# Kernel tuning notes

Measured on AMD Instinct MI355X. Metric: run time of the kernel, lower is better.

Reference implementation:

```python
import jax, jax.numpy as jnp
import numpy as np

EPS = 1e-5
SLOPE = 0.2
K = 20
B, N = 8, 2048

def _lrelu(x):
    return jnp.where(x >= 0, x, SLOPE * x)

def _bn(x, g, b, m, v, axis):
    # eval-mode batchnorm with running stats
    shape = [1] * x.ndim
    shape[axis] = -1
    g, b, m, v = (t.reshape(shape) for t in (g, b, m, v))
    return g * (x - m) * jax.lax.rsqrt(v + EPS) + b

def _knn(x, k):
    # x: (B, C, N) -> neighbor indices (B, N, k) by largest negative sq dist
    xx = jnp.sum(x * x, axis=1)                      # (B, N)
    inner = jnp.einsum('bcn,bcm->bnm', x, x)         # (B, N, N)
    pd = 2.0 * inner - xx[:, :, None] - xx[:, None, :]
    return jax.lax.top_k(pd, k)[1]

def _graph_feature(x, k):
    # x: (B, C, N) -> (B, 2C, N, k) edge features [nbr - center, center]
    idx = _knn(x, k)                                  # (B, N, k)
    xt = jnp.transpose(x, (0, 2, 1))                  # (B, N, C)
    nbr = xt[jnp.arange(x.shape[0])[:, None, None], idx]  # (B, N, k, C)
    center = xt[:, :, None, :]
    f = jnp.concatenate([nbr - center, jnp.broadcast_to(center, nbr.shape)], axis=-1)
    return jnp.transpose(f, (0, 3, 1, 2))

def _edge_block(x, W, g, b, m, v):
    f = _graph_feature(x, K)                          # (B, 2C, N, k)
    h = jnp.einsum('oc,bcnk->bonk', W, f)             # 1x1 conv
    return jnp.max(_lrelu(_bn(h, g, b, m, v, 1)), axis=-1)

def _forward(x, W1, bn1_g, bn1_b, bn1_m, bn1_v, W2, bn2_g, bn2_b, bn2_m, bn2_v, W3, bn3_g, bn3_b, bn3_m, bn3_v, W4, bn4_g, bn4_b, bn4_m, bn4_v, l1_w, l1_b, bn5_g, bn5_b, bn5_m, bn5_v, l2_w, l2_b, bn6_g, bn6_b, bn6_m, bn6_v, l3_w, l3_b):
    xc = jnp.transpose(x, (0, 2, 1))                  # (B, 3, N)
    x1 = _edge_block(xc, W1, bn1_g, bn1_b, bn1_m, bn1_v)   # (B, 64, N)
    x2 = _edge_block(x1, W2, bn2_g, bn2_b, bn2_m, bn2_v)   # (B, 64, N)
    x3 = _edge_block(x2, W3, bn3_g, bn3_b, bn3_m, bn3_v)   # (B, 128, N)
    h = jnp.concatenate([x1, x2, x3], axis=1)         # (B, 256, N)
    h = _lrelu(_bn(jnp.einsum('oc,bcn->bon', W4, h), bn4_g, bn4_b, bn4_m, bn4_v, 1))
    h = jnp.max(h, axis=-1)                           # (B, 1024)
    h = _lrelu(_bn(h @ l1_w.T + l1_b, bn5_g, bn5_b, bn5_m, bn5_v, 1))
    h = _lrelu(_bn(h @ l2_w.T + l2_b, bn6_g, bn6_b, bn6_m, bn6_v, 1))
    return h @ l3_w.T + l3_b                          # (B, 2)

def setup_inputs() -> dict:
    key = jax.random.key(0)
    ks = iter(jax.random.split(key, 64))
    def rn(shape, s=1.0):
        return jax.random.normal(next(ks), shape, jnp.float32) * s
    def add_bn(inp, prefix, c):
        inp[prefix + '_g'] = jax.random.uniform(next(ks), (c,), jnp.float32, 0.5, 1.5)
        inp[prefix + '_b'] = rn((c,), 0.1)
        inp[prefix + '_m'] = rn((c,), 0.1)
        inp[prefix + '_v'] = jax.random.uniform(next(ks), (c,), jnp.float32, 0.5, 1.5)
    inp = {'x': rn((B, N, 3))}
    inp['W1'] = rn((64, 6), 0.3); add_bn(inp, 'bn1', 64)
    inp['W2'] = rn((64, 128), 0.1); add_bn(inp, 'bn2', 64)
    inp['W3'] = rn((128, 128), 0.1); add_bn(inp, 'bn3', 128)
    inp['W4'] = rn((1024, 256), 0.08); add_bn(inp, 'bn4', 1024)
    inp['l1_w'] = rn((512, 1024), 0.03); inp['l1_b'] = rn((512,), 0.01); add_bn(inp, 'bn5', 512)
    inp['l2_w'] = rn((256, 512), 0.05); inp['l2_b'] = rn((256,), 0.01); add_bn(inp, 'bn6', 256)
    inp['l3_w'] = rn((2, 256), 0.06); inp['l3_b'] = rn((2,), 0.01)
    return inp

def reference(x, W1, bn1_g, bn1_b, bn1_m, bn1_v, W2, bn2_g, bn2_b, bn2_m, bn2_v, W3, bn3_g, bn3_b, bn3_m, bn3_v, W4, bn4_g, bn4_b, bn4_m, bn4_v, l1_w, l1_b, bn5_g, bn5_b, bn5_m, bn5_v, l2_w, l2_b, bn6_g, bn6_b, bn6_m, bn6_v, l3_w, l3_b):
    return _forward(x, W1, bn1_g, bn1_b, bn1_m, bn1_v, W2, bn2_g, bn2_b, bn2_m, bn2_v, W3, bn3_g, bn3_b, bn3_m, bn3_v, W4, bn4_g, bn4_b, bn4_m, bn4_v, l1_w, l1_b, bn5_g, bn5_b, bn5_m, bn5_v, l2_w, l2_b, bn6_g, bn6_b, bn6_m, bn6_v, l3_w, l3_b)
```

## Files before the change

kernel.cpp:

```cpp
#include <hip/hip_runtime.h>
#include <math.h>

#define NN 2048
#define KK 20
#define EPSF 1e-5f

__device__ __forceinline__ float lrelu(float v){ return v >= 0.f ? v : 0.2f*v; }

__device__ __forceinline__ void topk20_insert(float d, int idc, float (&v)[KK], int (&id)[KK]){
#pragma unroll
  for (int j = KK-1; j >= 1; --j){
    bool cjm1 = d > v[j-1];
    bool cj   = d > v[j];
    float nv = cjm1 ? v[j-1] : (cj ? d   : v[j]);
    int   ni = cjm1 ? id[j-1] : (cj ? idc : id[j]);
    v[j] = nv; id[j] = ni;
  }
  if (d > v[0]) { v[0] = d; id[0] = idc; }
}

__global__ void k_prep1(const float* __restrict__ x, const float* __restrict__ W1,
                        float* __restrict__ Y, float* __restrict__ T, float* __restrict__ SQ){
  __shared__ float wa[64][3], wd[64][3];
  int t = threadIdx.x;
  if (t < 64){
#pragma unroll
    for (int c=0;c<3;c++){
      float a = W1[t*6+c], b2 = W1[t*6+3+c];
      wa[t][c] = a; wd[t][c] = b2 - a;
    }
  }
  __syncthreads();
  int gid = blockIdx.x*256 + t;
  int b = gid >> 11, n = gid & (NN-1);
  float px = x[gid*3+0], py = x[gid*3+1], pz = x[gid*3+2];
  SQ[gid] = px*px + py*py + pz*pz;
  float* yb = Y + ((size_t)b*128)*NN + n;
  float* tb = T + ((size_t)b*128)*NN + n;
#pragma unroll 8
  for (int o=0;o<64;o++){
    yb[(size_t)o*NN] = wa[o][0]*px + wa[o][1]*py + wa[o][2]*pz;
    tb[(size_t)o*NN] = wd[o][0]*px + wd[o][1]*py + wd[o][2]*pz;
  }
}

__global__ __launch_bounds__(256) void k_knn3_part(const float* __restrict__ x, const float* __restrict__ SQ,
                                                   float* __restrict__ PV, unsigned short* __restrict__ PI){
  __shared__ __align__(16) float cd[128*4];
  int t = threadIdx.x;
  int half = blockIdx.x & 1, nb = blockIdx.x >> 1;
  int b = blockIdx.y;
  int n_base = nb * 32;
  int cbase = half * 1024;
  int ql = t & 31, sp = t >> 5;
  int n = n_base + ql;
  int gq = b*NN + n;
  float qx = x[gq*3], qy = x[gq*3+1], qz = x[gq*3+2];
  float qs = SQ[gq];
  float v[KK]; int id[KK];
#pragma unroll
  for (int i=0;i<KK;i++){ v[i] = -INFINITY; id[i] = 0; }
  int mlo = sp * 16;
  for (int tile=0; tile<8; ++tile){
    int m0 = cbase + tile * 128;
    __syncthreads();
#pragma unroll
    for (int i=0;i<2;i++){
      int f2 = t + i*256;
      int m = f2 >> 2, ch = f2 & 3;
      int gm = b*NN + m0 + m;
      cd[f2] = (ch < 3) ? x[gm*3 + ch] : SQ[gm];
    }
    __syncthreads();
    for (int j=mlo; j<mlo+16; ++j){
      float4 c4 = *(const float4*)&cd[j*4];
      float d = 2.f*(qx*c4.x + qy*c4.y + qz*c4.z) - qs - c4.w;
      if (d > v[KK-1]) topk20_insert(d, m0 + j, v, id);
    }
  }
  size_t base = ((size_t)b*16 + half*8 + sp)*KK;
#pragma unroll
  for (int r=0;r<KK;r++){
    PV[(base + r)*NN + n] = v[r];
    PI[(base + r)*NN + n] = (unsigned short)id[r];
  }
}

__global__ void k_sqnorm(const float* __restrict__ X, float* __restrict__ SQ){
  int gid = blockIdx.x*256 + threadIdx.x;
  int b = gid >> 11, n = gid & (NN-1);
  const float* xb = X + (size_t)b*256*NN;
  float s = 0.f;
#pragma unroll
  for (int c=0;c<64;c++){ float vv = xb[(size_t)c*NN + n]; s += vv*vv; }
  SQ[gid] = s;
}

__global__ __launch_bounds__(256) void k_gram(const float* __restrict__ X, float* __restrict__ D, int mh){
  __shared__ __align__(16) float am[32][132];
  __shared__ __align__(16) float bn[32][132];
  int t = threadIdx.x;
  int io = t >> 4, in_ = t & 15;
  int nb = blockIdx.x * 128;
  int mb = blockIdx.y * 128;
  int b = blockIdx.z;
  const float* xb = X + (size_t)b*256*NN;
  int mg = mh*1024 + mb;
  float acc[8][8];
#pragma unroll
  for (int r=0;r<8;r++)
#pragma unroll
    for (int c=0;c<8;c++) acc[r][c]=0.f;
  for (int c0=0; c0<64; c0+=32){
    __syncthreads();
#pragma unroll
    for (int p=0;p<4;p++){
      int idx = p*256 + t;
      int cc = idx >> 5, m4 = (idx & 31) * 4;
      *(float4*)&am[cc][m4] = *(const float4*)&xb[(size_t)(c0+cc)*NN + mg + m4];
    }
#pragma unroll
    for (int p=0;p<4;p++){
      int idx = p*256 + t;
      int cc = idx >> 5, n4 = (idx & 31) * 4;
      *(float4*)&bn[cc][n4] = *(const float4*)&xb[(size_t)(c0+cc)*NN + nb + n4];
    }
    __syncthreads();
#pragma unroll 4
    for (int c=0;c<32;c++){
      float4 a0 = *(const float4*)&am[c][io*8];
      float4 a1 = *(const float4*)&am[c][io*8+4];
      float4 b0 = *(const float4*)&bn[c][in_*8];
      float4 b1 = *(const float4*)&bn[c][in_*8+4];
      float ar[8] = {a0.x,a0.y,a0.z,a0.w,a1.x,a1.y,a1.z,a1.w};
      float br[8] = {b0.x,b0.y,b0.z,b0.w,b1.x,b1.y,b1.z,b1.w};
#pragma unroll
      for (int r=0;r<8;r++)
#pragma unroll
        for (int s=0;s<8;s++) acc[r][s] += ar[r]*br[s];
    }
  }
#pragma unroll
  for (int r=0;r<8;r++){
    size_t row = ((size_t)b*1024 + mb + io*8 + r)*NN + nb + in_*8;
    *(float4*)&D[row]   = make_float4(acc[r][0],acc[r][1],acc[r][2],acc[r][3]);
    *(float4*)&D[row+4] = make_float4(acc[r][4],acc[r][5],acc[r][6],acc[r][7]);
  }
}

__global__ __launch_bounds__(256) void k_sel1024(const float* __restrict__ D, const float* __restrict__ SQ,
                                                 int mh, float* __restrict__ PV, unsigned short* __restrict__ PI){
  int t = threadIdx.x;
  int q = t & 31, sp = t >> 5;
  int b = blockIdx.y;
  int n = blockIdx.x*32 + q;
  float qs = SQ[b*NN + n];
  const float* drow = D + ((size_t)b*1024 + sp*128)*NN + n;
  const float* sqb  = SQ + b*NN + mh*1024 + sp*128;
  int idb = mh*1024 + sp*128;
  float v[KK]; int id[KK];
#pragma unroll
  for (int i=0;i<KK;i++){ v[i]=-INFINITY; id[i]=0; }
  float dk[8];
#pragma unroll
  for (int k=0;k<8;k++) dk[k] = drow[(size_t)k*NN];
  for (int i=0;i<128;i+=8){
    float nk[8];
    if (i + 8 < 128){
#pragma unroll
      for (int k=0;k<8;k++) nk[k] = drow[(size_t)(i+8+k)*NN];
    }
#pragma unroll
    for (int k=0;k<8;k++){
      float d = 2.f*dk[k] - qs - sqb[i+k];
      if (d > v[KK-1]) topk20_insert(d, idb + i + k, v, id);
    }
#pragma unroll
    for (int k=0;k<8;k++) dk[k] = nk[k];
  }
  size_t base = ((size_t)b*16 + mh*8 + sp)*KK;
#pragma unroll
  for (int r=0;r<KK;r++){
    PV[(base + r)*NN + n] = v[r];
    PI[(base + r)*NN + n] = (unsigned short)id[r];
  }
}

__global__ void k_topk_merge16(const float* __restrict__ PV, const unsigned short* __restrict__ PI,
                               int* __restrict__ IDX){
  int gid = blockIdx.x*256 + threadIdx.x;
  int b = gid >> 11, n = gid & (NN-1);
  float hv[16]; int hi_[16]; int hp[16];
#pragma unroll
  for (int s=0;s<16;s++){
    hp[s] = 0;
    hv[s] = PV[(((size_t)b*16 + s)*KK)*NN + n];
    hi_[s] = (int)PI[(((size_t)b*16 + s)*KK)*NN + n];
  }
  for (int r=0;r<KK;r++){
    float bv = hv[0]; int bi = hi_[0]; int bs = 0;
#pragma unroll
    for (int s=1;s<16;s++){
      bool win = (hv[s] > bv) || ((hv[s] == bv) && (hi_[s] < bi));
      bv = win ? hv[s] : bv; bi = win ? hi_[s] : bi; bs = win ? s : bs;
    }
    IDX[((size_t)b*KK + r)*NN + n] = bi;
#pragma unroll
    for (int s=0;s<16;s++){
      if (s == bs){
        int np = hp[s] + 1; hp[s] = np;
        bool ok = np < KK;
        hv[s]  = ok ? PV[(((size_t)b*16 + s)*KK + np)*NN + n] : -INFINITY;
        hi_[s] = ok ? (int)PI[(((size_t)b*16 + s)*KK + np)*NN + n] : 0x7FFFFFFF;
      }
    }
  }
}

__global__ __launch_bounds__(256) void k_edge_apply(const float* __restrict__ Y, const float* __restrict__ T,
                             const int* __restrict__ IDX,
                             const float* __restrict__ g, const float* __restrict__ be,
                             const float* __restrict__ mu, const float* __restrict__ va,
                             float* __restrict__ OUT, int c_off){
  int t = threadIdx.x;
  int nl = t & 127, oh = t >> 7;
  int n = blockIdx.x*128 + nl;
  int b = blockIdx.z;
  int o0 = blockIdx.y*32 + oh*16;
  int idx[KK];
#pragma unroll
  for (int k2=0;k2<KK;k2++) idx[k2] = IDX[((size_t)b*KK + k2)*NN + n];
  for (int oo=0;oo<16;oo++){
    int o = o0 + oo;
    const float* yrow = Y + ((size_t)b*128 + o)*NN;
    float M = -INFINITY;
#pragma unroll
    for (int k2=0;k2<KK;k2++) M = fmaxf(M, yrow[idx[k2]]);
    float s = g[o] * rsqrtf(va[o] + EPSF);
    float val = s*(M + T[((size_t)b*128 + o)*NN + n] - mu[o]) + be[o];
    OUT[((size_t)b*256 + c_off + o)*NN + n] = lrelu(val);
  }
}

template<int O>
__global__ __launch_bounds__(256) void k_yt_gemm(const float* __restrict__ X, const float* __restrict__ W,
                                                 float* __restrict__ Y, float* __restrict__ T){
  __shared__ __align__(16) float wa[O][64];
  __shared__ __align__(16) float wd[O][64];
  int t = threadIdx.x;
  for (int i=t; i<O*64; i+=256){
    int o = i >> 6, c = i & 63;
    float a = W[o*128 + c];
    wa[o][c] = a;
    wd[o][c] = W[o*128 + 64 + c] - a;
  }
  __syncthreads();
  int half = t >> 7, ln = t & 127;
  int gid = blockIdx.x*128 + ln;
  int b = gid >> 11, n = gid & (NN-1);
  const float* xb = X + (size_t)b*256*NN;
  float q[64];
#pragma unroll
  for (int c=0;c<64;c++) q[c] = xb[(size_t)c*NN + n];
  int o0 = half * (O/2);
  for (int o=o0; o<o0+O/2; ++o){
    float ay=0.f, at=0.f;
#pragma unroll
    for (int c=0;c<64;c+=4){
      float4 a4 = *(const float4*)&wa[o][c];
      float4 d4 = *(const float4*)&wd[o][c];
      ay += a4.x*q[c] + a4.y*q[c+1] + a4.z*q[c+2] + a4.w*q[c+3];
      at += d4.x*q[c] + d4.y*q[c+1] + d4.z*q[c+2] + d4.w*q[c+3];
    }
    Y[((size_t)b*128 + o)*NN + n] = ay;
    T[((size_t)b*128 + o)*NN + n] = at;
  }
}

__global__ __launch_bounds__(256) void k_w4t(const float* __restrict__ W4, float* __restrict__ W4T){
  __shared__ float Tt[64][65];
  int t = threadIdx.x;
  int c0 = blockIdx.x * 64, o0 = blockIdx.y * 64;
#pragma unroll
  for (int p=0;p<16;p++){
    int f = p*256 + t;
    int i = f >> 6, j = f & 63;
    Tt[i][j] = W4[(size_t)(o0+i)*256 + c0 + j];
  }
  __syncthreads();
#pragma unroll
  for (int p=0;p<16;p++){
    int f = p*256 + t;
    int i = f >> 6, j = f & 63;
    W4T[(size_t)(c0+i)*1024 + o0 + j] = Tt[j][i];
  }
}

__global__ __launch_bounds__(256) void k_w4max(const float* __restrict__ CAT, const float* __restrict__ W4T,
                                               float* __restrict__ PART){
  __shared__ __align__(16) float wt[32][132];
  __shared__ __align__(16) float ct[32][132];
  int t = threadIdx.x;
  int io = t >> 4, in_ = t & 15;
  int nb = blockIdx.x * 128, ob = blockIdx.y * 128, b = blockIdx.z;
  const float* catb = CAT + (size_t)b*256*NN;
  float acc[8][8];
#pragma unroll
  for (int r=0;r<8;r++)
#pragma unroll
    for (int c=0;c<8;c++) acc[r][c]=0.f;
  for (int c0=0; c0<256; c0+=32){
    __syncthreads();
#pragma unroll
    for (int p=0;p<4;p++){
      int idx = p*256 + t;
      int cc = idx >> 5, o4 = (idx & 31) * 4;
      *(float4*)&wt[cc][o4] = *(const float4*)&W4T[(size_t)(c0+cc)*1024 + ob + o4];
    }
#pragma unroll
    for (int p=0;p<4;p++){
      int idx = p*256 + t;
      int cc = idx >> 5, n4 = (idx & 31) * 4;
      *(float4*)&ct[cc][n4] = *(const float4*)&catb[(size_t)(c0+cc)*NN + nb + n4];
    }
    __syncthreads();
#pragma unroll 4
    for (int c=0;c<32;c++){
      float4 a0 = *(const float4*)&wt[c][io*8];
      float4 a1 = *(const float4*)&wt[c][io*8+4];
      float4 b0 = *(const float4*)&ct[c][in_*8];
      float4 b1 = *(const float4*)&ct[c][in_*8+4];
      float ar[8] = {a0.x,a0.y,a0.z,a0.w,a1.x,a1.y,a1.z,a1.w};
      float br[8] = {b0.x,b0.y,b0.z,b0.w,b1.x,b1.y,b1.z,b1.w};
#pragma unroll
      for (int r=0;r<8;r++)
#pragma unroll
        for (int s=0;s<8;s++) acc[r][s] += ar[r]*br[s];
    }
  }
#pragma unroll
  for (int r=0;r<8;r++){
    float m = acc[r][0];
#pragma unroll
    for (int s=1;s<8;s++) m = fmaxf(m, acc[r][s]);
    m = fmaxf(m, __shfl_xor(m, 1));
    m = fmaxf(m, __shfl_xor(m, 2));
    m = fmaxf(m, __shfl_xor(m, 4));
    m = fmaxf(m, __shfl_xor(m, 8));
    if (in_ == 0){
      int o = ob + io*8 + r;
      PART[((size_t)b*1024 + o)*16 + blockIdx.x] = m;
    }
  }
}

__global__ void k_reduce4(const float* __restrict__ PART,
                          const float* __restrict__ g, const float* __restrict__ be,
                          const float* __restrict__ mu, const float* __restrict__ va,
                          float* __restrict__ H4){
  int gid = blockIdx.x*256 + threadIdx.x;
  int o = gid & 1023;
  float M = -INFINITY;
#pragma unroll
  for (int i=0;i<16;i++) M = fmaxf(M, PART[(size_t)gid*16 + i]);
  float s = g[o]*rsqrtf(va[o]+EPSF);
  H4[gid] = lrelu(s*(M - mu[o]) + be[o]);
}

__global__ __launch_bounds__(256) void k_mlp(const float* __restrict__ H4,
      const float* __restrict__ l1w, const float* __restrict__ l1b,
      const float* __restrict__ g5, const float* __restrict__ b5,
      const float* __restrict__ m5, const float* __restrict__ v5,
      const float* __restrict__ l2w, const float* __restrict__ l2b,
      const float* __restrict__ g6, const float* __restrict__ b6,
      const float* __restrict__ m6, const float* __restrict__ v6,
      const float* __restrict__ l3w, const float* __restrict__ l3b,
      float* __restrict__ out){
  __shared__ float h[1024];
  __shared__ float h5[512];
  __shared__ float h6[256];
  int b = blockIdx.x, t = threadIdx.x;
  for (int i=t;i<1024;i+=256) h[i] = H4[b*1024+i];
  __syncthreads();
  for (int o=t;o<512;o+=256){
    float acc = l1b[o];
    for (int c=0;c<1024;c+=4){
      float4 w = *(const float4*)&l1w[(size_t)o*1024 + c];
      acc += w.x*h[c] + w.y*h[c+1] + w.z*h[c+2] + w.w*h[c+3];
    }
    float s = g5[o]*rsqrtf(v5[o]+EPSF);
    h5[o] = lrelu(s*(acc - m5[o]) + b5[o]);
  }
  __syncthreads();
  if (t < 256){
    int o = t;
    float acc = l2b[o];
    for (int c=0;c<512;c+=4){
      float4 w = *(const float4*)&l2w[(size_t)o*512 + c];
      acc += w.x*h5[c] + w.y*h5[c+1] + w.z*h5[c+2] + w.w*h5[c+3];
    }
    float s = g6[o]*rsqrtf(v6[o]+EPSF);
    h6[o] = lrelu(s*(acc - m6[o]) + b6[o]);
  }
  __syncthreads();
  if (t < 128){
    int o = t >> 6, l = t & 63;
    float p = 0.f;
#pragma unroll
    for (int j=0;j<4;j++){ int c = j*64 + l; p += l3w[o*256 + c]*h6[c]; }
    p += __shfl_xor(p, 32); p += __shfl_xor(p, 16); p += __shfl_xor(p, 8);
    p += __shfl_xor(p, 4);  p += __shfl_xor(p, 2);  p += __shfl_xor(p, 1);
    if (l == 0) out[b*2 + o] = p + l3b[o];
  }
}

extern "C" void kernel_launch(void* const* d_in, const int* in_sizes, int n_in,
                              void* d_out, int out_size, void* d_ws, size_t ws_size,
                              hipStream_t stream){
  (void)in_sizes; (void)n_in; (void)out_size; (void)ws_size;
  const float* x    = (const float*)d_in[0];
  const float* W1   = (const float*)d_in[1];
  const float* bn1g = (const float*)d_in[2];
  const float* bn1b = (const float*)d_in[3];
  const float* bn1m = (const float*)d_in[4];
  const float* bn1v = (const float*)d_in[5];
  const float* W2   = (const float*)d_in[6];
  const float* bn2g = (const float*)d_in[7];
  const float* bn2b = (const float*)d_in[8];
  const float* bn2m = (const float*)d_in[9];
  const float* bn2v = (const float*)d_in[10];
  const float* W3   = (const float*)d_in[11];
  const float* bn3g = (const float*)d_in[12];
  const float* bn3b = (const float*)d_in[13];
  const float* bn3m = (const float*)d_in[14];
  const float* bn3v = (const float*)d_in[15];
  const float* W4   = (const float*)d_in[16];
  const float* bn4g = (const float*)d_in[17];
  const float* bn4b = (const float*)d_in[18];
  const float* bn4m = (const float*)d_in[19];
  const float* bn4v = (const float*)d_in[20];
  const float* l1w  = (const float*)d_in[21];
  const float* l1b  = (const float*)d_in[22];
  const float* bn5g = (const float*)d_in[23];
  const float* bn5b = (const float*)d_in[24];
  const float* bn5m = (const float*)d_in[25];
  const float* bn5v = (const float*)d_in[26];
  const float* l2w  = (const float*)d_in[27];
  const float* l2b  = (const float*)d_in[28];
  const float* bn6g = (const float*)d_in[29];
  const float* bn6b = (const float*)d_in[30];
  const float* bn6m = (const float*)d_in[31];
  const float* bn6v = (const float*)d_in[32];
  const float* l3w  = (const float*)d_in[33];
  const float* l3b  = (const float*)d_in[34];

  float* CAT  = (float*)d_ws;
  float* Yb   = CAT + (size_t)8*256*NN;
  float* Tb   = Yb  + (size_t)8*128*NN;
  float* SQ   = Tb  + (size_t)8*128*NN;
  int*   IDX  = (int*)(SQ + (size_t)8*NN);
  float* PART = (float*)(IDX + (size_t)8*KK*NN);
  float* H4   = PART + (size_t)8*1024*16;
  float* W4T  = H4 + (size_t)8*1024;
  float* PTV  = W4T + (size_t)256*1024;
  unsigned short* PTI = (unsigned short*)(PTV + (size_t)8*16*KK*NN);
  float* D    = (float*)(PTI + (size_t)8*16*KK*NN);

  k_w4t<<<dim3(4,16),256,0,stream>>>(W4, W4T);
  k_prep1<<<64,256,0,stream>>>(x, W1, Yb, Tb, SQ);
  k_knn3_part<<<dim3(128,8),256,0,stream>>>(x, SQ, PTV, PTI);
  k_topk_merge16<<<64,256,0,stream>>>(PTV, PTI, IDX);
  k_edge_apply<<<dim3(16,2,8),256,0,stream>>>(Yb, Tb, IDX, bn1g, bn1b, bn1m, bn1v, CAT, 0);
  k_sqnorm<<<64,256,0,stream>>>(CAT, SQ);
  k_gram<<<dim3(16,8,8),256,0,stream>>>(CAT, D, 0);
  k_sel1024<<<dim3(64,8),256,0,stream>>>(D, SQ, 0, PTV, PTI);
  k_gram<<<dim3(16,8,8),256,0,stream>>>(CAT, D, 1);
  k_sel1024<<<dim3(64,8),256,0,stream>>>(D, SQ, 1, PTV, PTI);
  k_topk_merge16<<<64,256,0,stream>>>(PTV, PTI, IDX);
  k_yt_gemm<64><<<128,256,0,stream>>>(CAT, W2, Yb, Tb);
  k_edge_apply<<<dim3(16,2,8),256,0,stream>>>(Yb, Tb, IDX, bn2g, bn2b, bn2m, bn2v, CAT, 64);
  k_sqnorm<<<64,256,0,stream>>>(CAT + (size_t)64*NN, SQ);
  k_gram<<<dim3(16,8,8),256,0,stream>>>(CAT + (size_t)64*NN, D, 0);
  k_sel1024<<<dim3(64,8),256,0,stream>>>(D, SQ, 0, PTV, PTI);
  k_gram<<<dim3(16,8,8),256,0,stream>>>(CAT + (size_t)64*NN, D, 1);
  k_sel1024<<<dim3(64,8),256,0,stream>>>(D, SQ, 1, PTV, PTI);
  k_topk_merge16<<<64,256,0,stream>>>(PTV, PTI, IDX);
  k_yt_gemm<128><<<128,256,0,stream>>>(CAT + (size_t)64*NN, W3, Yb, Tb);
  k_edge_apply<<<dim3(16,4,8),256,0,stream>>>(Yb, Tb, IDX, bn3g, bn3b, bn3m, bn3v, CAT, 128);
  k_w4max<<<dim3(16,8,8),256,0,stream>>>(CAT, W4T, PART);
  k_reduce4<<<32,256,0,stream>>>(PART, bn4g, bn4b, bn4m, bn4v, H4);
  k_mlp<<<8,256,0,stream>>>(H4, l1w, l1b, bn5g, bn5b, bn5m, bn5v,
                            l2w, l2b, bn6g, bn6b, bn6m, bn6v, l3w, l3b, (float*)d_out);
}
```

Measured before the change: 1.425 ms.

## Replace per-thread top-k insertion with wavefront bitonic sort and merge selection

Measured after the change: 1.429 ms. No clear change (+0.3%).

```diff
diff --git a/kernel.cpp b/kernel.cpp
--- a/kernel.cpp
+++ b/kernel.cpp
@@ -1,5 +1,6 @@
 #include <hip/hip_runtime.h>
 #include <math.h>
+#include <limits.h>
 
 #define NN 2048
 #define KK 20
@@ -7,16 +8,43 @@
 
 __device__ __forceinline__ float lrelu(float v){ return v >= 0.f ? v : 0.2f*v; }
 
-__device__ __forceinline__ void topk20_insert(float d, int idc, float (&v)[KK], int (&id)[KK]){
-#pragma unroll
-  for (int j = KK-1; j >= 1; --j){
-    bool cjm1 = d > v[j-1];
-    bool cj   = d > v[j];
-    float nv = cjm1 ? v[j-1] : (cj ? d   : v[j]);
-    int   ni = cjm1 ? id[j-1] : (cj ? idc : id[j]);
-    v[j] = nv; id[j] = ni;
-  }
-  if (d > v[0]) { v[0] = d; id[0] = idc; }
+__device__ __forceinline__ bool lexgt(float av, int ai, float bv, int bi){
+  return (av > bv) || ((av == bv) && (ai < bi));
+}
+
+__device__ __forceinline__ void bsort64(float &v, int &id, int lane){
+#pragma unroll
+  for (int k = 2; k <= 64; k <<= 1){
+#pragma unroll
+    for (int j = k >> 1; j > 0; j >>= 1){
+      float pv = __shfl_xor(v, j);
+      int   pid = __shfl_xor(id, j);
+      bool lower = (lane & j) == 0;
+      bool desc  = (lane & k) == 0;
+      bool mine_gt = lexgt(v, id, pv, pid);
+      bool keep = (lower == desc) ? mine_gt : !mine_gt;
+      v  = keep ? v  : pv;
+      id = keep ? id : pid;
+    }
+  }
+}
+
+__device__ __forceinline__ void bmerge64(float &rv, int &rid, float nv, int nid, int lane){
+  float xv  = __shfl(nv, 63 - lane);
+  int   xid = __shfl(nid, 63 - lane);
+  bool mine = lexgt(rv, rid, xv, xid);
+  rv  = mine ? rv  : xv;
+  rid = mine ? rid : xid;
+#pragma unroll
+  for (int j = 32; j > 0; j >>= 1){
+    float pv = __shfl_xor(rv, j);
+    int   pid = __shfl_xor(rid, j);
+    bool lower = (lane & j) == 0;
+    bool mine_gt = lexgt(rv, rid, pv, pid);
+    bool keep = lower ? mine_gt : !mine_gt;
+    rv  = keep ? rv  : pv;
+    rid = keep ? rid : pid;
+  }
 }
 
 __global__ void k_prep1(const float* __restrict__ x, const float* __restrict__ W1,
@@ -44,46 +72,36 @@
   }
 }
 
-__global__ __launch_bounds__(256) void k_knn3_part(const float* __restrict__ x, const float* __restrict__ SQ,
-                                                   float* __restrict__ PV, unsigned short* __restrict__ PI){
-  __shared__ __align__(16) float cd[128*4];
-  int t = threadIdx.x;
-  int half = blockIdx.x & 1, nb = blockIdx.x >> 1;
+__global__ __launch_bounds__(256) void k_knn3_bt(const float* __restrict__ x, const float* __restrict__ SQ,
+                                                 int* __restrict__ IDX){
+  __shared__ float cx[256], cy[256], cz[256], cq[256];
+  int t = threadIdx.x;
+  int lane = t & 63, w = t >> 6;
   int b = blockIdx.y;
-  int n_base = nb * 32;
-  int cbase = half * 1024;
-  int ql = t & 31, sp = t >> 5;
-  int n = n_base + ql;
+  int n = blockIdx.x*4 + w;
   int gq = b*NN + n;
   float qx = x[gq*3], qy = x[gq*3+1], qz = x[gq*3+2];
   float qs = SQ[gq];
-  float v[KK]; int id[KK];
-#pragma unroll
-  for (int i=0;i<KK;i++){ v[i] = -INFINITY; id[i] = 0; }
-  int mlo = sp * 16;
+  float rv = -INFINITY; int rid = INT_MAX;
   for (int tile=0; tile<8; ++tile){
-    int m0 = cbase + tile * 128;
-    __syncthreads();
-#pragma unroll
-    for (int i=0;i<2;i++){
-      int f2 = t + i*256;
-      int m = f2 >> 2, ch = f2 & 3;
-      int gm = b*NN + m0 + m;
-      cd[f2] = (ch < 3) ? x[gm*3 + ch] : SQ[gm];
-    }
-    __syncthreads();
-    for (int j=mlo; j<mlo+16; ++j){
-      float4 c4 = *(const float4*)&cd[j*4];
-      float d = 2.f*(qx*c4.x + qy*c4.y + qz*c4.z) - qs - c4.w;
-      if (d > v[KK-1]) topk20_insert(d, m0 + j, v, id);
-    }
-  }
-  size_t base = ((size_t)b*16 + half*8 + sp)*KK;
-#pragma unroll
-  for (int r=0;r<KK;r++){
-    PV[(base + r)*NN + n] = v[r];
-    PI[(base + r)*NN + n] = (unsigned short)id[r];
-  }
+    __syncthreads();
+    int m = tile*256 + t;
+    int gm = b*NN + m;
+    cx[t] = x[gm*3]; cy[t] = x[gm*3+1]; cz[t] = x[gm*3+2]; cq[t] = SQ[gm];
+    __syncthreads();
+#pragma unroll
+    for (int sb=0; sb<4; ++sb){
+      int ml = sb*64 + lane;
+      float d = 2.f*(qx*cx[ml] + qy*cy[ml] + qz*cz[ml]) - qs - cq[ml];
+      int idc = tile*256 + ml;
+      float t20v = __shfl(rv, 19); int t20i = __shfl(rid, 19);
+      if (__any(lexgt(d, idc, t20v, t20i))){
+        bsort64(d, idc, lane);
+        bmerge64(rv, rid, d, idc, lane);
+      }
+    }
+  }
+  if (lane < KK) IDX[((size_t)b*KK + lane)*NN + n] = rid;
 }
 
 __global__ void k_sqnorm(const float* __restrict__ X, float* __restrict__ SQ){
@@ -96,13 +114,13 @@
   SQ[gid] = s;
 }
 
-__global__ __launch_bounds__(256) void k_gram(const float* __restrict__ X, float* __restrict__ D, int mh){
-  __shared__ __align__(16) float am[32][132];
-  __shared__ __align__(16) float bn[32][132];
+__global__ __launch_bounds__(256) void k_gram(const float* __restrict__ X, float* __restrict__ Dt, int mh){
+  __shared__ __align__(16) float an[32][132];
+  __shared__ __align__(16) float bm[32][132];
   int t = threadIdx.x;
   int io = t >> 4, in_ = t & 15;
-  int nb = blockIdx.x * 128;
-  int mb = blockIdx.y * 128;
+  int mb = blockIdx.x * 128;
+  int nb = blockIdx.y * 128;
   int b = blockIdx.z;
   const float* xb = X + (size_t)b*256*NN;
   int mg = mh*1024 + mb;
@@ -116,22 +134,22 @@
 #pragma unroll
     for (int p=0;p<4;p++){
       int idx = p*256 + t;
-      int cc = idx >> 5, m4 = (idx & 31) * 4;
-      *(float4*)&am[cc][m4] = *(const float4*)&xb[(size_t)(c0+cc)*NN + mg + m4];
+      int cc = idx >> 5, n4 = (idx & 31) * 4;
+      *(float4*)&an[cc][n4] = *(const float4*)&xb[(size_t)(c0+cc)*NN + nb + n4];
     }
 #pragma unroll
     for (int p=0;p<4;p++){
       int idx = p*256 + t;
-      int cc = idx >> 5, n4 = (idx & 31) * 4;
-      *(float4*)&bn[cc][n4] = *(const float4*)&xb[(size_t)(c0+cc)*NN + nb + n4];
+      int cc = idx >> 5, m4 = (idx & 31) * 4;
+      *(float4*)&bm[cc][m4] = *(const float4*)&xb[(size_t)(c0+cc)*NN + mg + m4];
     }
     __syncthreads();
 #pragma unroll 4
     for (int c=0;c<32;c++){
-      float4 a0 = *(const float4*)&am[c][io*8];
-      float4 a1 = *(const float4*)&am[c][io*8+4];
-      float4 b0 = *(const float4*)&bn[c][in_*8];
-      float4 b1 = *(const float4*)&bn[c][in_*8+4];
+      float4 a0 = *(const float4*)&an[c][io*8];
+      float4 a1 = *(const float4*)&an[c][io*8+4];
+      float4 b0 = *(const float4*)&bm[c][in_*8];
+      float4 b1 = *(const float4*)&bm[c][in_*8+4];
       float ar[8] = {a0.x,a0.y,a0.z,a0.w,a1.x,a1.y,a1.z,a1.w};
       float br[8] = {b0.x,b0.y,b0.z,b0.w,b1.x,b1.y,b1.z,b1.w};
 #pragma unroll
@@ -142,78 +160,47 @@
   }
 #pragma unroll
   for (int r=0;r<8;r++){
-    size_t row = ((size_t)b*1024 + mb + io*8 + r)*NN + nb + in_*8;
-    *(float4*)&D[row]   = make_float4(acc[r][0],acc[r][1],acc[r][2],acc[r][3]);
-    *(float4*)&D[row+4] = make_float4(acc[r][4],acc[r][5],acc[r][6],acc[r][7]);
-  }
-}
-
-__global__ __launch_bounds__(256) void k_sel1024(const float* __restrict__ D, const float* __restrict__ SQ,
-                                                 int mh, float* __restrict__ PV, unsigned short* __restrict__ PI){
-  int t = threadIdx.x;
-  int q = t & 31, sp = t >> 5;
+    size_t row = ((size_t)b*NN + nb + io*8 + r)*1024 + mb + in_*8;
+    *(float4*)&Dt[row]   = make_float4(acc[r][0],acc[r][1],acc[r][2],acc[r][3]);
+    *(float4*)&Dt[row+4] = make_float4(acc[r][4],acc[r][5],acc[r][6],acc[r][7]);
+  }
+}
+
+__global__ __launch_bounds__(256) void k_sel_bt(const float* __restrict__ Dt, const float* __restrict__ SQ,
+                                                int mh, int phase,
+                                                float* __restrict__ RV, int* __restrict__ RI,
+                                                int* __restrict__ IDX){
+  int t = threadIdx.x;
+  int lane = t & 63, w = t >> 6;
   int b = blockIdx.y;
-  int n = blockIdx.x*32 + q;
+  int n = blockIdx.x*4 + w;
   float qs = SQ[b*NN + n];
-  const float* drow = D + ((size_t)b*1024 + sp*128)*NN + n;
-  const float* sqb  = SQ + b*NN + mh*1024 + sp*128;
-  int idb = mh*1024 + sp*128;
-  float v[KK]; int id[KK];
-#pragma unroll
-  for (int i=0;i<KK;i++){ v[i]=-INFINITY; id[i]=0; }
-  float dk[8];
-#pragma unroll
-  for (int k=0;k<8;k++) dk[k] = drow[(size_t)k*NN];
-  for (int i=0;i<128;i+=8){
-    float nk[8];
-    if (i + 8 < 128){
-#pragma unroll
-      for (int k=0;k<8;k++) nk[k] = drow[(size_t)(i+8+k)*NN];
-    }
-#pragma unroll
-    for (int k=0;k<8;k++){
-      float d = 2.f*dk[k] - qs - sqb[i+k];
-      if (d > v[KK-1]) topk20_insert(d, idb + i + k, v, id);
-    }
-#pragma unroll
-    for (int k=0;k<8;k++) dk[k] = nk[k];
-  }
-  size_t base = ((size_t)b*16 + mh*8 + sp)*KK;
-#pragma unroll
-  for (int r=0;r<KK;r++){
-    PV[(base + r)*NN + n] = v[r];
-    PI[(base + r)*NN + n] = (unsigned short)id[r];
-  }
-}
-
-__global__ void k_topk_merge16(const float* __restrict__ PV, const unsigned short* __restrict__ PI,
-                               int* __restrict__ IDX){
-  int gid = blockIdx.x*256 + threadIdx.x;
-  int b = gid >> 11, n = gid & (NN-1);
-  float hv[16]; int hi_[16]; int hp[16];
-#pragma unroll
-  for (int s=0;s<16;s++){
-    hp[s] = 0;
-    hv[s] = PV[(((size_t)b*16 + s)*KK)*NN + n];
-    hi_[s] = (int)PI[(((size_t)b*16 + s)*KK)*NN + n];
-  }
-  for (int r=0;r<KK;r++){
-    float bv = hv[0]; int bi = hi_[0]; int bs = 0;
-#pragma unroll
-    for (int s=1;s<16;s++){
-      bool win = (hv[s] > bv) || ((hv[s] == bv) && (hi_[s] < bi));
-      bv = win ? hv[s] : bv; bi = win ? hi_[s] : bi; bs = win ? s : bs;
-    }
-    IDX[((size_t)b*KK + r)*NN + n] = bi;
-#pragma unroll
-    for (int s=0;s<16;s++){
-      if (s == bs){
-        int np = hp[s] + 1; hp[s] = np;
-        bool ok = np < KK;
-        hv[s]  = ok ? PV[(((size_t)b*16 + s)*KK + np)*NN + n] : -INFINITY;
-        hi_[s] = ok ? (int)PI[(((size_t)b*16 + s)*KK + np)*NN + n] : 0x7FFFFFFF;
-      }
-    }
+  float rv; int rid;
+  if (phase == 0){ rv = -INFINITY; rid = INT_MAX; }
+  else {
+    if (lane < KK){ rv = RV[((size_t)b*NN + n)*KK + lane]; rid = RI[((size_t)b*NN + n)*KK + lane]; }
+    else          { rv = -INFINITY; rid = INT_MAX; }
+  }
+  const float* drow = Dt + ((size_t)b*NN + n)*1024;
+  const float* sqh  = SQ + b*NN + mh*1024;
+#pragma unroll
+  for (int sb=0; sb<16; ++sb){
+    int ml = sb*64 + lane;
+    float d = 2.f*drow[ml] - qs - sqh[ml];
+    int idc = mh*1024 + ml;
+    float t20v = __shfl(rv, 19); int t20i = __shfl(rid, 19);
+    if (__any(lexgt(d, idc, t20v, t20i))){
+      bsort64(d, idc, lane);
+      bmerge64(rv, rid, d, idc, lane);
+    }
+  }
+  if (phase == 0){
+    if (lane < KK){
+      RV[((size_t)b*NN + n)*KK + lane] = rv;
+      RI[((size_t)b*NN + n)*KK + lane] = rid;
+    }
+  } else {
+    if (lane < KK) IDX[((size_t)b*KK + lane)*NN + n] = rid;
   }
 }
 
@@ -462,29 +449,26 @@
   float* PART = (float*)(IDX + (size_t)8*KK*NN);
   float* H4   = PART + (size_t)8*1024*16;
   float* W4T  = H4 + (size_t)8*1024;
-  float* PTV  = W4T + (size_t)256*1024;
-  unsigned short* PTI = (unsigned short*)(PTV + (size_t)8*16*KK*NN);
-  float* D    = (float*)(PTI + (size_t)8*16*KK*NN);
+  float* RV   = W4T + (size_t)256*1024;
+  int*   RI   = (int*)(RV + (size_t)8*NN*KK);
+  float* Dt   = (float*)(RI + (size_t)8*NN*KK);
 
   k_w4t<<<dim3(4,16),256,0,stream>>>(W4, W4T);
   k_prep1<<<64,256,0,stream>>>(x, W1, Yb, Tb, SQ);
-  k_knn3_part<<<dim3(128,8),256,0,stream>>>(x, SQ, PTV, PTI);
-  k_topk_merge16<<<64,256,0,stream>>>(PTV, PTI, IDX);
+  k_knn3_bt<<<dim3(512,8),256,0,stream>>>(x, SQ, IDX);
   k_edge_apply<<<dim3(16,2,8),256,0,stream>>>(Yb, Tb, IDX, bn1g, bn1b, bn1m, bn1v, CAT, 0);
   k_sqnorm<<<64,256,0,stream>>>(CAT, SQ);
-  k_gram<<<dim3(16,8,8),256,0,stream>>>(CAT, D, 0);
-  k_sel1024<<<dim3(64,8),256,0,stream>>>(D, SQ, 0, PTV, PTI);
-  k_gram<<<dim3(16,8,8),256,0,stream>>>(CAT, D, 1);
-  k_sel1024<<<dim3(64,8),256,0,stream>>>(D, SQ, 1, PTV, PTI);
-  k_topk_merge16<<<64,256,0,stream>>>(PTV, PTI, IDX);
+  k_gram<<<dim3(8,16,8),256,0,stream>>>(CAT, Dt, 0);
+  k_sel_bt<<<dim3(512,8),256,0,stream>>>(Dt, SQ, 0, 0, RV, RI, IDX);
+  k_gram<<<dim3(8,16,8),256,0,stream>>>(CAT, Dt, 1);
+  k_sel_bt<<<dim3(512,8),256,0,stream>>>(Dt, SQ, 1, 1, RV, RI, IDX);
   k_yt_gemm<64><<<128,256,0,stream>>>(CAT, W2, Yb, Tb);
   k_edge_apply<<<dim3(16,2,8),256,0,stream>>>(Yb, Tb, IDX, bn2g, bn2b, bn2m, bn2v, CAT, 64);
   k_sqnorm<<<64,256,0,stream>>>(CAT + (size_t)64*NN, SQ);
-  k_gram<<<dim3(16,8,8),256,0,stream>>>(CAT + (size_t)64*NN, D, 0);
-  k_sel1024<<<dim3(64,8),256,0,stream>>>(D, SQ, 0, PTV, PTI);
-  k_gram<<<dim3(16,8,8),256,0,stream>>>(CAT + (size_t)64*NN, D, 1);
-  k_sel1024<<<dim3(64,8),256,0,stream>>>(D, SQ, 1, PTV, PTI);
-  k_topk_merge16<<<64,256,0,stream>>>(PTV, PTI, IDX);
+  k_gram<<<dim3(8,16,8),256,0,stream>>>(CAT + (size_t)64*NN, Dt, 0);
+  k_sel_bt<<<dim3(512,8),256,0,stream>>>(Dt, SQ, 0, 0, RV, RI, IDX);
+  k_gram<<<dim3(8,16,8),256,0,stream>>>(CAT + (size_t)64*NN, Dt, 1);
+  k_sel_bt<<<dim3(512,8),256,0,stream>>>(Dt, SQ, 1, 1, RV, RI, IDX);
   k_yt_gemm<128><<<128,256,0,stream>>>(CAT + (size_t)64*NN, W3, Yb, Tb);
   k_edge_apply<<<dim3(16,4,8),256,0,stream>>>(Yb, Tb, IDX, bn3g, bn3b, bn3m, bn3v, CAT, 128);
   k_w4max<<<dim3(16,8,8),256,0,stream>>>(CAT, W4T, PART);
```
